# Kernel optimization log

Hardware: AMD Instinct MI355X
Metric: run time of the kernel (lower is better)

The kernel has to match this reference:

```python
import jax, jax.numpy as jnp
import numpy as np

N_NODES = 50000
N_EDGES = 800000
HID = 64
F_NODE = 64
F_EDGE = 16
DEC_H = 64
EPS = 1e-5


def setup_inputs() -> dict:
    key = jax.random.key(0)
    ks = jax.random.split(key, 16)
    inp = {}
    inp['x'] = jax.random.normal(ks[0], (N_NODES, F_NODE), dtype=jnp.float32)
    inp['edge_index'] = jax.random.randint(ks[1], (2, N_EDGES), 0, N_NODES, dtype=jnp.int32)
    inp['edge_attr'] = jax.random.normal(ks[2], (N_EDGES, F_EDGE), dtype=jnp.float32)
    # 3 GCN layers (F_NODE == HID so weights stack)
    inp['conv_w'] = jax.random.normal(ks[3], (3, HID, HID), dtype=jnp.float32) / np.sqrt(HID)
    inp['conv_b'] = jnp.zeros((3, HID), dtype=jnp.float32)
    inp['ln_g'] = jnp.ones((3, HID), dtype=jnp.float32)
    inp['ln_b'] = jnp.zeros((3, HID), dtype=jnp.float32)
    dec_in = 2 * HID + F_EDGE
    inp['dec_w1'] = jax.random.normal(ks[4], (dec_in, DEC_H), dtype=jnp.float32) / np.sqrt(dec_in)
    inp['dec_b1'] = jnp.zeros((DEC_H,), dtype=jnp.float32)
    inp['dec_w2'] = jax.random.normal(ks[5], (DEC_H, DEC_H // 2), dtype=jnp.float32) / np.sqrt(DEC_H)
    inp['dec_b2'] = jnp.zeros((DEC_H // 2,), dtype=jnp.float32)
    inp['dec_w3'] = jax.random.normal(ks[6], (DEC_H // 2, 1), dtype=jnp.float32) / np.sqrt(DEC_H // 2)
    inp['dec_b3'] = jnp.zeros((1,), dtype=jnp.float32)
    return inp


def _layer_norm(h, g, b):
    mu = jnp.mean(h, axis=-1, keepdims=True)
    var = jnp.mean(jnp.square(h - mu), axis=-1, keepdims=True)
    return (h - mu) * jax.lax.rsqrt(var + EPS) * g + b


def _forward(x, edge_index, edge_attr, conv_w, conv_b, ln_g, ln_b,
             dec_w1, dec_b1, dec_w2, dec_b2, dec_w3, dec_b3):
    n = x.shape[0]
    src, dst = edge_index[0], edge_index[1]
    # add self-loops (PyG GCNConv default)
    loop = jnp.arange(n, dtype=edge_index.dtype)
    src_sl = jnp.concatenate([src, loop])
    dst_sl = jnp.concatenate([dst, loop])
    # symmetric normalization: deg over target column (incl. self-loops)
    deg = jax.ops.segment_sum(jnp.ones_like(src_sl, dtype=x.dtype), dst_sl, num_segments=n)
    dinv = jnp.where(deg > 0, jax.lax.rsqrt(deg), 0.0)
    norm = dinv[src_sl] * dinv[dst_sl]  # (E+N,)

    h = x
    for l in range(conv_w.shape[0]):
        t = h @ conv_w[l]                                   # (N, H)
        msg = t[src_sl] * norm[:, None]                     # (E+N, H)
        agg = jax.ops.segment_sum(msg, dst_sl, num_segments=n) + conv_b[l]
        h = jax.nn.relu(_layer_norm(agg, ln_g[l], ln_b[l]))
        # dropout is identity at inference

    # edge decoder: concat(src_emb, dst_emb, edge_attr) -> MLP -> scalar
    z = jnp.concatenate([h[src], h[dst], edge_attr], axis=-1)  # (E, 2H+Fe)
    z = jax.nn.relu(z @ dec_w1 + dec_b1)
    z = jax.nn.relu(z @ dec_w2 + dec_b2)
    return (z @ dec_w3 + dec_b3).squeeze(-1)                   # (E,)


def reference(x, edge_index, edge_attr, conv_w, conv_b, ln_g, ln_b,
              dec_w1, dec_b1, dec_w2, dec_b2, dec_w3, dec_b3):
    return _forward(x, edge_index, edge_attr, conv_w, conv_b, ln_g, ln_b,
                    dec_w1, dec_b1, dec_w2, dec_b2, dec_w3, dec_b3)
```

## Files before the change

### kernel.cpp

```cpp
#include <hip/hip_runtime.h>
#include <hip/hip_fp16.h>

#define N_NODES 50000
#define N_EDGES 800000
#define HID 64
#define F_EDGE 16
#define LN_EPS 1e-5f
#define SCAN_BLOCKS ((N_NODES + 255) / 256)

typedef _Float16 h2n __attribute__((ext_vector_type(2)));

__device__ inline h2n to_n(__half2 v) {
    union { __half2 a; h2n b; } u; u.a = v; return u.b;
}
__device__ inline h2n pack2(float x, float y) {
    h2n r; r.x = (_Float16)x; r.y = (_Float16)y; return r;
}

__device__ inline float wave_sum64(float v) {
    #pragma unroll
    for (int o = 32; o > 0; o >>= 1) v += __shfl_xor(v, o, 64);
    return v;
}

__global__ void k_zero_cnt(int* __restrict__ cnt) {
    int i = blockIdx.x * blockDim.x + threadIdx.x;
    if (i < N_NODES) cnt[i] = 0;
}

__global__ void k_count(const int* __restrict__ dst, int* __restrict__ cnt) {
    int e = blockIdx.x * blockDim.x + threadIdx.x;
    if (e < N_EDGES) atomicAdd(&cnt[dst[e]], 1);
}

__global__ void k_scan1(const int* __restrict__ cnt, int* __restrict__ row_ptr,
                        int* __restrict__ bsum, float* __restrict__ dinv) {
    __shared__ int wsum[4];
    int tid = threadIdx.x, lane = tid & 63, w = tid >> 6;
    int i = blockIdx.x * 256 + tid;
    int v = (i < N_NODES) ? cnt[i] : 0;
    if (i < N_NODES) dinv[i] = rsqrtf((float)v + 1.0f);
    int isc = v;
    #pragma unroll
    for (int o = 1; o < 64; o <<= 1) {
        int n = __shfl_up(isc, o, 64);
        if (lane >= o) isc += n;
    }
    if (lane == 63) wsum[w] = isc;
    __syncthreads();
    int woff = 0;
    #pragma unroll
    for (int k = 0; k < 4; k++) woff += (k < w) ? wsum[k] : 0;
    if (i < N_NODES) row_ptr[i] = woff + isc - v;
    if (tid == 255) bsum[blockIdx.x] = woff + isc;
}

__global__ void k_scan2_prep(const int* __restrict__ bsum, int* __restrict__ boff,
                             const float* __restrict__ W1c, const float* __restrict__ W2,
                             __half2* __restrict__ w1cp, __half2* __restrict__ w2p) {
    __shared__ int wsum[4];
    int tid = threadIdx.x, lane = tid & 63, w = tid >> 6;
    int v = (tid < SCAN_BLOCKS) ? bsum[tid] : 0;
    int isc = v;
    #pragma unroll
    for (int o = 1; o < 64; o <<= 1) {
        int n = __shfl_up(isc, o, 64);
        if (lane >= o) isc += n;
    }
    if (lane == 63) wsum[w] = isc;
    __syncthreads();
    int woff = 0;
    #pragma unroll
    for (int k = 0; k < 4; k++) woff += (k < w) ? wsum[k] : 0;
    if (tid < SCAN_BLOCKS) boff[tid] = woff + isc - v;
    for (int i = tid; i < 8 * 64; i += 256) {
        int k2 = i >> 6, j = i & 63;
        w1cp[i] = __floats2half2_rn(W1c[(2 * k2) * 64 + j], W1c[(2 * k2 + 1) * 64 + j]);
    }
    for (int i = tid; i < 32 * 32; i += 256) {
        int k2 = i >> 5, j = i & 31;
        w2p[i] = __floats2half2_rn(W2[(2 * k2) * 32 + j], W2[(2 * k2 + 1) * 32 + j]);
    }
}

__global__ void k_scan3(int* __restrict__ row_ptr, const int* __restrict__ boff,
                        int* __restrict__ cursor) {
    int i = blockIdx.x * blockDim.x + threadIdx.x;
    if (i < N_NODES) {
        int r = row_ptr[i] + boff[i >> 8];
        row_ptr[i] = r;
        cursor[i] = r;
    }
    if (i == 0) row_ptr[N_NODES] = N_EDGES;
}

__global__ void k_fill(const int* __restrict__ src, const int* __restrict__ dst,
                       int* __restrict__ cursor, int* __restrict__ col) {
    int e = blockIdx.x * blockDim.x + threadIdx.x;
    if (e < N_EDGES) {
        int s = src[e], d = dst[e];
        int pos = atomicAdd(&cursor[d], 1);
        col[pos] = s;
    }
}

__global__ void k_xs_init(const float* __restrict__ x, const float* __restrict__ dinv,
                          __half* __restrict__ xs) {
    int i = blockIdx.x * blockDim.x + threadIdx.x;
    if (i < N_NODES * 64) xs[i] = __float2half_rn(x[i] * dinv[i >> 6]);
}

__device__ inline void row_acc(float4 raw, float m, float acc[8]) {
    const __half2* hp = (const __half2*)&raw;
    float2 f0 = __half22float2(hp[0]);
    float2 f1 = __half22float2(hp[1]);
    float2 f2 = __half22float2(hp[2]);
    float2 f3 = __half22float2(hp[3]);
    acc[0] = fmaf(f0.x, m, acc[0]); acc[1] = fmaf(f0.y, m, acc[1]);
    acc[2] = fmaf(f1.x, m, acc[2]); acc[3] = fmaf(f1.y, m, acc[3]);
    acc[4] = fmaf(f2.x, m, acc[4]); acc[5] = fmaf(f2.y, m, acc[5]);
    acc[6] = fmaf(f3.x, m, acc[6]); acc[7] = fmaf(f3.y, m, acc[7]);
}

__global__ void __launch_bounds__(256)
k_gather_agg(const __half* __restrict__ xs, const float* __restrict__ dinv,
             const int* __restrict__ row_ptr, const int* __restrict__ col,
             float* __restrict__ agg) {
    int gid = blockIdx.x * blockDim.x + threadIdx.x;
    int n = gid >> 3;
    if (n >= N_NODES) return;
    int c8 = gid & 7;
    const float4* x4 = (const float4*)xs;

    float acc[8];
    {
        float4 raw = x4[(size_t)n * 8 + c8];
        const __half2* hp = (const __half2*)&raw;
        float2 f0 = __half22float2(hp[0]);
        float2 f1 = __half22float2(hp[1]);
        float2 f2 = __half22float2(hp[2]);
        float2 f3 = __half22float2(hp[3]);
        acc[0] = f0.x; acc[1] = f0.y; acc[2] = f1.x; acc[3] = f1.y;
        acc[4] = f2.x; acc[5] = f2.y; acc[6] = f3.x; acc[7] = f3.y;
    }

    int beg = row_ptr[n], end = row_ptr[n + 1];
    int t = beg;
    int s0 = 0, s1 = 0, s2 = 0, s3 = 0;
    if (t < end) {
        int e1 = end - 1;
        s0 = col[t];
        s1 = col[min(t + 1, e1)];
        s2 = col[min(t + 2, e1)];
        s3 = col[min(t + 3, e1)];
    }
    while (t < end) {
        float m1 = (t + 1 < end) ? 1.0f : 0.0f;
        float m2 = (t + 2 < end) ? 1.0f : 0.0f;
        float m3 = (t + 3 < end) ? 1.0f : 0.0f;
        float4 r0 = x4[(size_t)s0 * 8 + c8];
        float4 r1 = x4[(size_t)s1 * 8 + c8];
        float4 r2 = x4[(size_t)s2 * 8 + c8];
        float4 r3 = x4[(size_t)s3 * 8 + c8];
        t += 4;
        if (t < end) {
            int e1 = end - 1;
            s0 = col[t];
            s1 = col[min(t + 1, e1)];
            s2 = col[min(t + 2, e1)];
            s3 = col[min(t + 3, e1)];
        }
        row_acc(r0, 1.0f, acc);
        row_acc(r1, m1, acc);
        row_acc(r2, m2, acc);
        row_acc(r3, m3, acc);
    }

    float di = dinv[n];
    float4 y0, y1;
    y0.x = acc[0] * di; y0.y = acc[1] * di; y0.z = acc[2] * di; y0.w = acc[3] * di;
    y1.x = acc[4] * di; y1.y = acc[5] * di; y1.z = acc[6] * di; y1.w = acc[7] * di;
    float4* a4 = (float4*)agg;
    a4[(size_t)n * 16 + 2 * c8] = y0;
    a4[(size_t)n * 16 + 2 * c8 + 1] = y1;
}

__global__ void __launch_bounds__(256)
k_gemm_ln(const float* __restrict__ agg, const float* __restrict__ W,
          const float* __restrict__ cb, const float* __restrict__ g,
          const float* __restrict__ b, const float* __restrict__ dinv,
          __half* __restrict__ xs_out, float* __restrict__ h_out) {
    int lane = threadIdx.x & 63;
    int wid = (blockIdx.x * blockDim.x + threadIdx.x) >> 6;
    int nwaves = (gridDim.x * blockDim.x) >> 6;
    float w[64];
    #pragma unroll
    for (int k = 0; k < 64; k++) w[k] = W[k * 64 + lane];
    float cbl = cb[lane], gl = g[lane], bl = b[lane];
    for (int row = wid; row < N_NODES; row += nwaves) {
        int r = __builtin_amdgcn_readfirstlane(row);
        const float* xr = agg + r * 64;
        float acc = cbl;
        #pragma unroll
        for (int k = 0; k < 64; k++) acc = fmaf(xr[k], w[k], acc);
        float mu = wave_sum64(acc) * (1.0f / 64.0f);
        float d = acc - mu;
        float var = wave_sum64(d * d) * (1.0f / 64.0f);
        float y = fmaxf(fmaf(d * rsqrtf(var + LN_EPS), gl, bl), 0.0f);
        if (xs_out) {
            xs_out[r * 64 + lane] = __float2half_rn(y * dinv[r]);
        } else {
            h_out[r * 64 + lane] = y;
        }
    }
}

__global__ void __launch_bounds__(256)
k_gemm_pq(const float* __restrict__ hin, const float* __restrict__ Wp,
          const float* __restrict__ bp, const float* __restrict__ Wq,
          __half* __restrict__ P, __half* __restrict__ Q) {
    int half_g = gridDim.x >> 1;
    bool isQ = (blockIdx.x >= half_g);
    const float* W = isQ ? Wq : Wp;
    __half* out = isQ ? Q : P;
    int lane = threadIdx.x & 63;
    int bid = isQ ? (blockIdx.x - half_g) : blockIdx.x;
    int wid = (bid * blockDim.x + threadIdx.x) >> 6;
    int nwaves = (half_g * blockDim.x) >> 6;
    float w[64];
    #pragma unroll
    for (int k = 0; k < 64; k++) w[k] = W[k * 64 + lane];
    float binit = isQ ? 0.0f : bp[lane];
    for (int row = wid; row < N_NODES; row += nwaves) {
        int r = __builtin_amdgcn_readfirstlane(row);
        const float* xr = hin + r * 64;
        float acc = binit;
        #pragma unroll
        for (int k = 0; k < 64; k++) acc = fmaf(xr[k], w[k], acc);
        out[r * 64 + lane] = __float2half_rn(acc);
    }
}

__global__ void __launch_bounds__(256)
k_decoder(const __half* __restrict__ P, const __half* __restrict__ Q,
          const int* __restrict__ src, const int* __restrict__ dst,
          const float* __restrict__ attr,
          const __half2* __restrict__ w1cp,
          const __half2* __restrict__ w2p, const float* __restrict__ b2,
          const float* __restrict__ W3, const float* __restrict__ b3,
          float* __restrict__ out) {
    int e = blockIdx.x * blockDim.x + threadIdx.x;
    if (e >= N_EDGES) return;
    int s = src[e], d = dst[e];

    const float4* ap = (const float4*)(attr + (size_t)e * 16);
    float4 av0 = ap[0], av1 = ap[1], av2 = ap[2], av3 = ap[3];
    h2n a2[8];
    a2[0] = pack2(av0.x, av0.y); a2[1] = pack2(av0.z, av0.w);
    a2[2] = pack2(av1.x, av1.y); a2[3] = pack2(av1.z, av1.w);
    a2[4] = pack2(av2.x, av2.y); a2[5] = pack2(av2.z, av2.w);
    a2[6] = pack2(av3.x, av3.y); a2[7] = pack2(av3.z, av3.w);

    float acc[64];
    const float4* Pp = (const float4*)(P + (size_t)s * 64);
    const float4* Qp = (const float4*)(Q + (size_t)d * 64);
    #pragma unroll
    for (int c = 0; c < 8; c++) {
        float4 pv = Pp[c], qv = Qp[c];
        const __half2* ph = (const __half2*)&pv;
        const __half2* qh = (const __half2*)&qv;
        #pragma unroll
        for (int u = 0; u < 4; u++) {
            float2 pf = __half22float2(ph[u]);
            float2 qf = __half22float2(qh[u]);
            acc[8 * c + 2 * u]     = pf.x + qf.x;
            acc[8 * c + 2 * u + 1] = pf.y + qf.y;
        }
    }

    #pragma unroll
    for (int k2 = 0; k2 < 8; k2++) {
        #pragma unroll
        for (int j = 0; j < 64; j++)
            acc[j] = __builtin_amdgcn_fdot2(a2[k2], to_n(w1cp[k2 * 64 + j]), acc[j], false);
    }

    h2n hh[32];
    #pragma unroll
    for (int k2 = 0; k2 < 32; k2++)
        hh[k2] = pack2(fmaxf(acc[2 * k2], 0.0f), fmaxf(acc[2 * k2 + 1], 0.0f));

    float acc2[32];
    #pragma unroll
    for (int j = 0; j < 32; j++) acc2[j] = b2[j];
    #pragma unroll
    for (int k2 = 0; k2 < 32; k2++) {
        #pragma unroll
        for (int j = 0; j < 32; j++)
            acc2[j] = __builtin_amdgcn_fdot2(hh[k2], to_n(w2p[k2 * 32 + j]), acc2[j], false);
    }

    float o = b3[0];
    #pragma unroll
    for (int j = 0; j < 32; j++)
        o = fmaf(fmaxf(acc2[j], 0.0f), W3[j], o);
    out[e] = o;
}

extern "C" void kernel_launch(void* const* d_in, const int* in_sizes, int n_in,
                              void* d_out, int out_size, void* d_ws, size_t ws_size,
                              hipStream_t stream) {
    const float* x      = (const float*)d_in[0];
    const int*   ei     = (const int*)d_in[1];
    const float* attr   = (const float*)d_in[2];
    const float* conv_w = (const float*)d_in[3];
    const float* conv_b = (const float*)d_in[4];
    const float* ln_g   = (const float*)d_in[5];
    const float* ln_b   = (const float*)d_in[6];
    const float* dw1    = (const float*)d_in[7];
    const float* db1    = (const float*)d_in[8];
    const float* dw2    = (const float*)d_in[9];
    const float* db2    = (const float*)d_in[10];
    const float* dw3    = (const float*)d_in[11];
    const float* db3    = (const float*)d_in[12];
    float* out = (float*)d_out;

    const int* src = ei;
    const int* dst = ei + N_EDGES;

    char* p = (char*)d_ws;
    float*   dinv    = (float*)p;   p += sizeof(float) * N_NODES;
    float*   agg     = (float*)p;   p += sizeof(float) * (size_t)N_NODES * 64;
    float*   h3      = (float*)p;   p += sizeof(float) * (size_t)N_NODES * 64;
    __half*  xs      = (__half*)p;  p += sizeof(__half) * (size_t)N_NODES * 64;
    __half*  P_h     = (__half*)p;  p += sizeof(__half) * (size_t)N_NODES * 64;
    __half*  Q_h     = (__half*)p;  p += sizeof(__half) * (size_t)N_NODES * 64;
    int*     cnt     = (int*)p;     p += sizeof(int) * N_NODES;
    int*     cursor  = (int*)p;     p += sizeof(int) * N_NODES;
    int*     row_ptr = (int*)p;     p += sizeof(int) * (N_NODES + 1);
    int*     col     = (int*)p;     p += sizeof(int) * N_EDGES;
    int*     bsum    = (int*)p;     p += sizeof(int) * 256;
    int*     boff    = (int*)p;     p += sizeof(int) * 256;
    __half2* w1cp    = (__half2*)p; p += sizeof(__half2) * 8 * 64;
    __half2* w2p     = (__half2*)p; p += sizeof(__half2) * 32 * 32;

    const int nb_nodes = (N_NODES + 255) / 256;
    const int nb_edges = (N_EDGES + 255) / 256;
    const int nb_elems = (N_NODES * 64 + 255) / 256;

    k_zero_cnt<<<nb_nodes, 256, 0, stream>>>(cnt);
    k_count<<<nb_edges, 256, 0, stream>>>(dst, cnt);
    k_scan1<<<SCAN_BLOCKS, 256, 0, stream>>>(cnt, row_ptr, bsum, dinv);
    k_scan2_prep<<<1, 256, 0, stream>>>(bsum, boff, dw1 + 128 * 64, dw2, w1cp, w2p);
    k_scan3<<<nb_nodes, 256, 0, stream>>>(row_ptr, boff, cursor);
    k_fill<<<nb_edges, 256, 0, stream>>>(src, dst, cursor, col);
    k_xs_init<<<nb_elems, 256, 0, stream>>>(x, dinv, xs);

    const int gemm_blocks = 1024;
    const int gather_blocks = (N_NODES * 8 + 255) / 256;

    for (int l = 0; l < 3; l++) {
        k_gather_agg<<<gather_blocks, 256, 0, stream>>>(xs, dinv, row_ptr, col, agg);
        bool last = (l == 2);
        k_gemm_ln<<<gemm_blocks, 256, 0, stream>>>(
            agg, conv_w + l * 4096, conv_b + l * 64,
            ln_g + l * 64, ln_b + l * 64, dinv,
            last ? (__half*)nullptr : xs, last ? h3 : (float*)nullptr);
    }

    k_gemm_pq<<<2 * gemm_blocks, 256, 0, stream>>>(h3, dw1, db1, dw1 + 64 * 64, P_h, Q_h);

    k_decoder<<<nb_edges, 256, 0, stream>>>(
        P_h, Q_h, src, dst, attr, w1cp, w2p, db2, dw3, db3, out);
}
```

Baseline: 438.8 us.

## Process decoder edges in CSR order and fuse setup kernels

The decoder now walks edges in destination-sorted CSR order, using a new eid permutation array written by k_fill, so Q rows (by dst) are reused across neighbouring threads and gathers get better cache locality. Attr reads and output writes become scattered through eid, which is the cost paid for that locality. The xs initialisation is folded into the scan3 kernel and the count-zeroing kernel is replaced by a memset, cutting two launches.

```diff
diff --git a/kernel.cpp b/kernel.cpp
--- a/kernel.cpp
+++ b/kernel.cpp
@@ -21,11 +21,6 @@
     #pragma unroll
     for (int o = 32; o > 0; o >>= 1) v += __shfl_xor(v, o, 64);
     return v;
-}
-
-__global__ void k_zero_cnt(int* __restrict__ cnt) {
-    int i = blockIdx.x * blockDim.x + threadIdx.x;
-    if (i < N_NODES) cnt[i] = 0;
 }
 
 __global__ void k_count(const int* __restrict__ dst, int* __restrict__ cnt) {
@@ -83,8 +78,10 @@
     }
 }
 
-__global__ void k_scan3(int* __restrict__ row_ptr, const int* __restrict__ boff,
-                        int* __restrict__ cursor) {
+__global__ void k_scan3_xs(int* __restrict__ row_ptr, const int* __restrict__ boff,
+                           int* __restrict__ cursor,
+                           const float* __restrict__ x, const float* __restrict__ dinv,
+                           __half* __restrict__ xs) {
     int i = blockIdx.x * blockDim.x + threadIdx.x;
     if (i < N_NODES) {
         int r = row_ptr[i] + boff[i >> 8];
@@ -92,22 +89,19 @@
         cursor[i] = r;
     }
     if (i == 0) row_ptr[N_NODES] = N_EDGES;
+    if (i < N_NODES * 64) xs[i] = __float2half_rn(x[i] * dinv[i >> 6]);
 }
 
 __global__ void k_fill(const int* __restrict__ src, const int* __restrict__ dst,
-                       int* __restrict__ cursor, int* __restrict__ col) {
+                       int* __restrict__ cursor, int* __restrict__ col,
+                       int* __restrict__ eid) {
     int e = blockIdx.x * blockDim.x + threadIdx.x;
     if (e < N_EDGES) {
         int s = src[e], d = dst[e];
         int pos = atomicAdd(&cursor[d], 1);
         col[pos] = s;
-    }
-}
-
-__global__ void k_xs_init(const float* __restrict__ x, const float* __restrict__ dinv,
-                          __half* __restrict__ xs) {
-    int i = blockIdx.x * blockDim.x + threadIdx.x;
-    if (i < N_NODES * 64) xs[i] = __float2half_rn(x[i] * dinv[i >> 6]);
+        eid[pos] = e;
+    }
 }
 
 __device__ inline void row_acc(float4 raw, float m, float acc[8]) {
@@ -243,15 +237,18 @@
 
 __global__ void __launch_bounds__(256)
 k_decoder(const __half* __restrict__ P, const __half* __restrict__ Q,
-          const int* __restrict__ src, const int* __restrict__ dst,
+          const int* __restrict__ col, const int* __restrict__ eid,
+          const int* __restrict__ dst,
           const float* __restrict__ attr,
           const __half2* __restrict__ w1cp,
           const __half2* __restrict__ w2p, const float* __restrict__ b2,
           const float* __restrict__ W3, const float* __restrict__ b3,
           float* __restrict__ out) {
-    int e = blockIdx.x * blockDim.x + threadIdx.x;
-    if (e >= N_EDGES) return;
-    int s = src[e], d = dst[e];
+    int p = blockIdx.x * blockDim.x + threadIdx.x;
+    if (p >= N_EDGES) return;
+    int s = col[p];
+    int e = eid[p];
+    int d = dst[e];
 
     const float4* ap = (const float4*)(attr + (size_t)e * 16);
     float4 av0 = ap[0], av1 = ap[1], av2 = ap[2], av3 = ap[3];
@@ -339,22 +336,21 @@
     int*     cursor  = (int*)p;     p += sizeof(int) * N_NODES;
     int*     row_ptr = (int*)p;     p += sizeof(int) * (N_NODES + 1);
     int*     col     = (int*)p;     p += sizeof(int) * N_EDGES;
+    int*     eid     = (int*)p;     p += sizeof(int) * N_EDGES;
     int*     bsum    = (int*)p;     p += sizeof(int) * 256;
     int*     boff    = (int*)p;     p += sizeof(int) * 256;
     __half2* w1cp    = (__half2*)p; p += sizeof(__half2) * 8 * 64;
     __half2* w2p     = (__half2*)p; p += sizeof(__half2) * 32 * 32;
 
-    const int nb_nodes = (N_NODES + 255) / 256;
     const int nb_edges = (N_EDGES + 255) / 256;
     const int nb_elems = (N_NODES * 64 + 255) / 256;
 
-    k_zero_cnt<<<nb_nodes, 256, 0, stream>>>(cnt);
+    hipMemsetAsync(cnt, 0, sizeof(int) * N_NODES, stream);
     k_count<<<nb_edges, 256, 0, stream>>>(dst, cnt);
     k_scan1<<<SCAN_BLOCKS, 256, 0, stream>>>(cnt, row_ptr, bsum, dinv);
     k_scan2_prep<<<1, 256, 0, stream>>>(bsum, boff, dw1 + 128 * 64, dw2, w1cp, w2p);
-    k_scan3<<<nb_nodes, 256, 0, stream>>>(row_ptr, boff, cursor);
-    k_fill<<<nb_edges, 256, 0, stream>>>(src, dst, cursor, col);
-    k_xs_init<<<nb_elems, 256, 0, stream>>>(x, dinv, xs);
+    k_scan3_xs<<<nb_elems, 256, 0, stream>>>(row_ptr, boff, cursor, x, dinv, xs);
+    k_fill<<<nb_edges, 256, 0, stream>>>(src, dst, cursor, col, eid);
 
     const int gemm_blocks = 1024;
     const int gather_blocks = (N_NODES * 8 + 255) / 256;
@@ -371,5 +367,5 @@
     k_gemm_pq<<<2 * gemm_blocks, 256, 0, stream>>>(h3, dw1, db1, dw1 + 64 * 64, P_h, Q_h);
 
     k_decoder<<<nb_edges, 256, 0, stream>>>(
-        P_h, Q_h, src, dst, attr, w1cp, w2p, db2, dw3, db3, out);
-}
+        P_h, Q_h, col, eid, dst, attr, w1cp, w2p, db2, dw3, db3, out);
+}
```

Measured after the change: 437.0 us. No clear change (-0.4%).

## Split neighbor gather into two source-range passes for cache locality

Applied to the files above, without the earlier changes.

Each node's CSR row is partitioned by source index (below or above the midpoint), recorded with a packed high/low count and a second fill cursor. Aggregation then runs as two passes, each touching only half of the feature table, so that the gathered working set fits better in cache. The second pass reloads the partial sums and applies the normalization. Separately, the count zeroing is replaced by a memset and the xs init is fused into the scan3 kernel. The cost is an extra launch per layer and an extra read/write of agg.

```diff
diff --git a/kernel.cpp b/kernel.cpp
--- a/kernel.cpp
+++ b/kernel.cpp
@@ -3,12 +3,14 @@
 
 #define N_NODES 50000
 #define N_EDGES 800000
+#define MID 25000
 #define HID 64
 #define F_EDGE 16
 #define LN_EPS 1e-5f
 #define SCAN_BLOCKS ((N_NODES + 255) / 256)
 
 typedef _Float16 h2n __attribute__((ext_vector_type(2)));
+typedef float f4 __attribute__((ext_vector_type(4)));
 
 __device__ inline h2n to_n(__half2 v) {
     union { __half2 a; h2n b; } u; u.a = v; return u.b;
@@ -23,14 +25,13 @@
     return v;
 }
 
-__global__ void k_zero_cnt(int* __restrict__ cnt) {
-    int i = blockIdx.x * blockDim.x + threadIdx.x;
-    if (i < N_NODES) cnt[i] = 0;
-}
-
-__global__ void k_count(const int* __restrict__ dst, int* __restrict__ cnt) {
+__global__ void k_count(const int* __restrict__ src, const int* __restrict__ dst,
+                        int* __restrict__ cnt) {
     int e = blockIdx.x * blockDim.x + threadIdx.x;
-    if (e < N_EDGES) atomicAdd(&cnt[dst[e]], 1);
+    if (e < N_EDGES) {
+        int s = src[e], d = dst[e];
+        atomicAdd(&cnt[d], (s < MID) ? 0x10001 : 1);
+    }
 }
 
 __global__ void k_scan1(const int* __restrict__ cnt, int* __restrict__ row_ptr,
@@ -38,7 +39,7 @@
     __shared__ int wsum[4];
     int tid = threadIdx.x, lane = tid & 63, w = tid >> 6;
     int i = blockIdx.x * 256 + tid;
-    int v = (i < N_NODES) ? cnt[i] : 0;
+    int v = (i < N_NODES) ? (cnt[i] & 0xffff) : 0;
     if (i < N_NODES) dinv[i] = rsqrtf((float)v + 1.0f);
     int isc = v;
     #pragma unroll
@@ -83,31 +84,35 @@
     }
 }
 
-__global__ void k_scan3(int* __restrict__ row_ptr, const int* __restrict__ boff,
-                        int* __restrict__ cursor) {
+__global__ void k_scan3_xs(int* __restrict__ row_ptr, const int* __restrict__ boff,
+                           const int* __restrict__ cnt,
+                           int* __restrict__ cursor, int* __restrict__ cursor2,
+                           int* __restrict__ split,
+                           const float* __restrict__ x, const float* __restrict__ dinv,
+                           __half* __restrict__ xs) {
     int i = blockIdx.x * blockDim.x + threadIdx.x;
     if (i < N_NODES) {
         int r = row_ptr[i] + boff[i >> 8];
         row_ptr[i] = r;
         cursor[i] = r;
+        int sp = r + (cnt[i] >> 16);
+        split[i] = sp;
+        cursor2[i] = sp;
     }
     if (i == 0) row_ptr[N_NODES] = N_EDGES;
+    if (i < N_NODES * 64) xs[i] = __float2half_rn(x[i] * dinv[i >> 6]);
 }
 
 __global__ void k_fill(const int* __restrict__ src, const int* __restrict__ dst,
-                       int* __restrict__ cursor, int* __restrict__ col) {
+                       int* __restrict__ cursor, int* __restrict__ cursor2,
+                       int* __restrict__ col) {
     int e = blockIdx.x * blockDim.x + threadIdx.x;
     if (e < N_EDGES) {
         int s = src[e], d = dst[e];
-        int pos = atomicAdd(&cursor[d], 1);
+        int pos = (s < MID) ? atomicAdd(&cursor[d], 1)
+                            : atomicAdd(&cursor2[d], 1);
         col[pos] = s;
     }
-}
-
-__global__ void k_xs_init(const float* __restrict__ x, const float* __restrict__ dinv,
-                          __half* __restrict__ xs) {
-    int i = blockIdx.x * blockDim.x + threadIdx.x;
-    if (i < N_NODES * 64) xs[i] = __float2half_rn(x[i] * dinv[i >> 6]);
 }
 
 __device__ inline void row_acc(float4 raw, float m, float acc[8]) {
@@ -124,16 +129,20 @@
 
 __global__ void __launch_bounds__(256)
 k_gather_agg(const __half* __restrict__ xs, const float* __restrict__ dinv,
-             const int* __restrict__ row_ptr, const int* __restrict__ col,
-             float* __restrict__ agg) {
+             const int* __restrict__ row_ptr, const int* __restrict__ split,
+             const int* __restrict__ col, float* __restrict__ agg, int pass) {
     int gid = blockIdx.x * blockDim.x + threadIdx.x;
     int n = gid >> 3;
     if (n >= N_NODES) return;
     int c8 = gid & 7;
     const float4* x4 = (const float4*)xs;
 
+    int beg, end; bool self;
+    if (pass == 0) { beg = row_ptr[n]; end = split[n];       self = (n <  MID); }
+    else           { beg = split[n];   end = row_ptr[n + 1]; self = (n >= MID); }
+
     float acc[8];
-    {
+    if (self) {
         float4 raw = x4[(size_t)n * 8 + c8];
         const __half2* hp = (const __half2*)&raw;
         float2 f0 = __half22float2(hp[0]);
@@ -142,9 +151,11 @@
         float2 f3 = __half22float2(hp[3]);
         acc[0] = f0.x; acc[1] = f0.y; acc[2] = f1.x; acc[3] = f1.y;
         acc[4] = f2.x; acc[5] = f2.y; acc[6] = f3.x; acc[7] = f3.y;
-    }
-
-    int beg = row_ptr[n], end = row_ptr[n + 1];
+    } else {
+        #pragma unroll
+        for (int u = 0; u < 8; u++) acc[u] = 0.0f;
+    }
+
     int t = beg;
     int s0 = 0, s1 = 0, s2 = 0, s3 = 0;
     if (t < end) {
@@ -176,13 +187,26 @@
         row_acc(r3, m3, acc);
     }
 
-    float di = dinv[n];
-    float4 y0, y1;
-    y0.x = acc[0] * di; y0.y = acc[1] * di; y0.z = acc[2] * di; y0.w = acc[3] * di;
-    y1.x = acc[4] * di; y1.y = acc[5] * di; y1.z = acc[6] * di; y1.w = acc[7] * di;
-    float4* a4 = (float4*)agg;
-    a4[(size_t)n * 16 + 2 * c8] = y0;
-    a4[(size_t)n * 16 + 2 * c8 + 1] = y1;
+    f4* a4 = (f4*)agg;
+    size_t base = (size_t)n * 16 + 2 * c8;
+    if (pass == 0) {
+        f4 y0, y1;
+        y0.x = acc[0]; y0.y = acc[1]; y0.z = acc[2]; y0.w = acc[3];
+        y1.x = acc[4]; y1.y = acc[5]; y1.z = acc[6]; y1.w = acc[7];
+        __builtin_nontemporal_store(y0, &a4[base]);
+        __builtin_nontemporal_store(y1, &a4[base + 1]);
+    } else {
+        f4 p0 = __builtin_nontemporal_load(&a4[base]);
+        f4 p1 = __builtin_nontemporal_load(&a4[base + 1]);
+        float di = dinv[n];
+        f4 y0, y1;
+        y0.x = (acc[0] + p0.x) * di; y0.y = (acc[1] + p0.y) * di;
+        y0.z = (acc[2] + p0.z) * di; y0.w = (acc[3] + p0.w) * di;
+        y1.x = (acc[4] + p1.x) * di; y1.y = (acc[5] + p1.y) * di;
+        y1.z = (acc[6] + p1.z) * di; y1.w = (acc[7] + p1.w) * di;
+        a4[base] = y0;
+        a4[base + 1] = y1;
+    }
 }
 
 __global__ void __launch_bounds__(256)
@@ -337,6 +361,8 @@
     __half*  Q_h     = (__half*)p;  p += sizeof(__half) * (size_t)N_NODES * 64;
     int*     cnt     = (int*)p;     p += sizeof(int) * N_NODES;
     int*     cursor  = (int*)p;     p += sizeof(int) * N_NODES;
+    int*     cursor2 = (int*)p;     p += sizeof(int) * N_NODES;
+    int*     split   = (int*)p;     p += sizeof(int) * N_NODES;
     int*     row_ptr = (int*)p;     p += sizeof(int) * (N_NODES + 1);
     int*     col     = (int*)p;     p += sizeof(int) * N_EDGES;
     int*     bsum    = (int*)p;     p += sizeof(int) * 256;
@@ -344,23 +370,23 @@
     __half2* w1cp    = (__half2*)p; p += sizeof(__half2) * 8 * 64;
     __half2* w2p     = (__half2*)p; p += sizeof(__half2) * 32 * 32;
 
-    const int nb_nodes = (N_NODES + 255) / 256;
     const int nb_edges = (N_EDGES + 255) / 256;
     const int nb_elems = (N_NODES * 64 + 255) / 256;
 
-    k_zero_cnt<<<nb_nodes, 256, 0, stream>>>(cnt);
-    k_count<<<nb_edges, 256, 0, stream>>>(dst, cnt);
+    (void)hipMemsetAsync(cnt, 0, sizeof(int) * N_NODES, stream);
+    k_count<<<nb_edges, 256, 0, stream>>>(src, dst, cnt);
     k_scan1<<<SCAN_BLOCKS, 256, 0, stream>>>(cnt, row_ptr, bsum, dinv);
     k_scan2_prep<<<1, 256, 0, stream>>>(bsum, boff, dw1 + 128 * 64, dw2, w1cp, w2p);
-    k_scan3<<<nb_nodes, 256, 0, stream>>>(row_ptr, boff, cursor);
-    k_fill<<<nb_edges, 256, 0, stream>>>(src, dst, cursor, col);
-    k_xs_init<<<nb_elems, 256, 0, stream>>>(x, dinv, xs);
+    k_scan3_xs<<<nb_elems, 256, 0, stream>>>(row_ptr, boff, cnt, cursor, cursor2,
+                                             split, x, dinv, xs);
+    k_fill<<<nb_edges, 256, 0, stream>>>(src, dst, cursor, cursor2, col);
 
     const int gemm_blocks = 1024;
     const int gather_blocks = (N_NODES * 8 + 255) / 256;
 
     for (int l = 0; l < 3; l++) {
-        k_gather_agg<<<gather_blocks, 256, 0, stream>>>(xs, dinv, row_ptr, col, agg);
+        k_gather_agg<<<gather_blocks, 256, 0, stream>>>(xs, dinv, row_ptr, split, col, agg, 0);
+        k_gather_agg<<<gather_blocks, 256, 0, stream>>>(xs, dinv, row_ptr, split, col, agg, 1);
         bool last = (l == 2);
         k_gemm_ln<<<gemm_blocks, 256, 0, stream>>>(
             agg, conv_w + l * 4096, conv_b + l * 64,
```

New measurement: 483.6 us. 10.2% more time.

## Fuse GCN gather-aggregate with GEMM+LayerNorm per layer via LDS tile

Applied to the files above, without the earlier changes.

Merges the per-layer neighbor gather-aggregate kernel and the dense GEMM+LayerNorm kernel into one kernel. Each wave aggregates 8 nodes into a swizzled shared-memory tile, then runs the 64x64 matvec and LayerNorm from that tile. This removes the float32 agg round trip through global memory and three launches, and ping-pongs between two half-precision feature buffers. It also folds the xs initialisation into the scan3 kernel and replaces the zero kernel with a memset. In exchange, every wave now reloads all 64 weight columns per 8 rows, which raises register pressure and per-row load overhead.

```diff
diff --git a/kernel.cpp b/kernel.cpp
--- a/kernel.cpp
+++ b/kernel.cpp
@@ -21,11 +21,6 @@
     #pragma unroll
     for (int o = 32; o > 0; o >>= 1) v += __shfl_xor(v, o, 64);
     return v;
-}
-
-__global__ void k_zero_cnt(int* __restrict__ cnt) {
-    int i = blockIdx.x * blockDim.x + threadIdx.x;
-    if (i < N_NODES) cnt[i] = 0;
 }
 
 __global__ void k_count(const int* __restrict__ dst, int* __restrict__ cnt) {
@@ -83,8 +78,10 @@
     }
 }
 
-__global__ void k_scan3(int* __restrict__ row_ptr, const int* __restrict__ boff,
-                        int* __restrict__ cursor) {
+__global__ void k_scan3_xs(int* __restrict__ row_ptr, const int* __restrict__ boff,
+                           int* __restrict__ cursor,
+                           const float* __restrict__ x, const float* __restrict__ dinv,
+                           __half* __restrict__ xs) {
     int i = blockIdx.x * blockDim.x + threadIdx.x;
     if (i < N_NODES) {
         int r = row_ptr[i] + boff[i >> 8];
@@ -92,6 +89,7 @@
         cursor[i] = r;
     }
     if (i == 0) row_ptr[N_NODES] = N_EDGES;
+    if (i < N_NODES * 64) xs[i] = __float2half_rn(x[i] * dinv[i >> 6]);
 }
 
 __global__ void k_fill(const int* __restrict__ src, const int* __restrict__ dst,
@@ -102,12 +100,6 @@
         int pos = atomicAdd(&cursor[d], 1);
         col[pos] = s;
     }
-}
-
-__global__ void k_xs_init(const float* __restrict__ x, const float* __restrict__ dinv,
-                          __half* __restrict__ xs) {
-    int i = blockIdx.x * blockDim.x + threadIdx.x;
-    if (i < N_NODES * 64) xs[i] = __float2half_rn(x[i] * dinv[i >> 6]);
 }
 
 __device__ inline void row_acc(float4 raw, float m, float acc[8]) {
@@ -123,14 +115,20 @@
 }
 
 __global__ void __launch_bounds__(256)
-k_gather_agg(const __half* __restrict__ xs, const float* __restrict__ dinv,
-             const int* __restrict__ row_ptr, const int* __restrict__ col,
-             float* __restrict__ agg) {
-    int gid = blockIdx.x * blockDim.x + threadIdx.x;
-    int n = gid >> 3;
-    if (n >= N_NODES) return;
-    int c8 = gid & 7;
-    const float4* x4 = (const float4*)xs;
+k_layer(const __half* __restrict__ xs_in, const float* __restrict__ dinv,
+        const int* __restrict__ row_ptr, const int* __restrict__ col,
+        const float* __restrict__ W, const float* __restrict__ cb,
+        const float* __restrict__ gW, const float* __restrict__ bW,
+        __half* __restrict__ xs_out, float* __restrict__ h_out) {
+    __shared__ __align__(16) float tile[4][8 * 68];
+    int tid = threadIdx.x;
+    int wv = tid >> 6, lane = tid & 63;
+    int base = (blockIdx.x * 4 + wv) * 8;
+    if (base >= N_NODES) return;
+    int g8 = lane >> 3;
+    int c8 = lane & 7;
+    int n = base + g8;
+    const float4* x4 = (const float4*)xs_in;
 
     float acc[8];
     {
@@ -143,7 +141,6 @@
         acc[0] = f0.x; acc[1] = f0.y; acc[2] = f1.x; acc[3] = f1.y;
         acc[4] = f2.x; acc[5] = f2.y; acc[6] = f3.x; acc[7] = f3.y;
     }
-
     int beg = row_ptr[n], end = row_ptr[n + 1];
     int t = beg;
     int s0 = 0, s1 = 0, s2 = 0, s3 = 0;
@@ -176,41 +173,46 @@
         row_acc(r3, m3, acc);
     }
 
-    float di = dinv[n];
-    float4 y0, y1;
-    y0.x = acc[0] * di; y0.y = acc[1] * di; y0.z = acc[2] * di; y0.w = acc[3] * di;
-    y1.x = acc[4] * di; y1.y = acc[5] * di; y1.z = acc[6] * di; y1.w = acc[7] * di;
-    float4* a4 = (float4*)agg;
-    a4[(size_t)n * 16 + 2 * c8] = y0;
-    a4[(size_t)n * 16 + 2 * c8 + 1] = y1;
-}
-
-__global__ void __launch_bounds__(256)
-k_gemm_ln(const float* __restrict__ agg, const float* __restrict__ W,
-          const float* __restrict__ cb, const float* __restrict__ g,
-          const float* __restrict__ b, const float* __restrict__ dinv,
-          __half* __restrict__ xs_out, float* __restrict__ h_out) {
-    int lane = threadIdx.x & 63;
-    int wid = (blockIdx.x * blockDim.x + threadIdx.x) >> 6;
-    int nwaves = (gridDim.x * blockDim.x) >> 6;
+    {
+        float di = dinv[n];
+        float4 y0, y1;
+        y0.x = acc[0] * di; y0.y = acc[1] * di; y0.z = acc[2] * di; y0.w = acc[3] * di;
+        y1.x = acc[4] * di; y1.y = acc[5] * di; y1.z = acc[6] * di; y1.w = acc[7] * di;
+        float4* rowv = (float4*)&tile[wv][g8 * 68];
+        rowv[(2 * c8)     ^ (g8 << 1)] = y0;
+        rowv[(2 * c8 + 1) ^ (g8 << 1)] = y1;
+    }
+
     float w[64];
     #pragma unroll
     for (int k = 0; k < 64; k++) w[k] = W[k * 64 + lane];
-    float cbl = cb[lane], gl = g[lane], bl = b[lane];
-    for (int row = wid; row < N_NODES; row += nwaves) {
-        int r = __builtin_amdgcn_readfirstlane(row);
-        const float* xr = agg + r * 64;
-        float acc = cbl;
-        #pragma unroll
-        for (int k = 0; k < 64; k++) acc = fmaf(xr[k], w[k], acc);
-        float mu = wave_sum64(acc) * (1.0f / 64.0f);
-        float d = acc - mu;
+    float cbl = cb[lane], gl = gW[lane], bl = bW[lane];
+    #pragma unroll
+    for (int r = 0; r < 8; r++) {
+        const float4* rw = (const float4*)&tile[wv][r * 68];
+        float a = cbl;
+        #pragma unroll
+        for (int j = 0; j < 8; j++) {
+            float4 p0 = rw[(2 * j)     ^ (r << 1)];
+            float4 p1 = rw[(2 * j + 1) ^ (r << 1)];
+            a = fmaf(p0.x, w[j * 8 + 0], a);
+            a = fmaf(p0.y, w[j * 8 + 1], a);
+            a = fmaf(p0.z, w[j * 8 + 2], a);
+            a = fmaf(p0.w, w[j * 8 + 3], a);
+            a = fmaf(p1.x, w[j * 8 + 4], a);
+            a = fmaf(p1.y, w[j * 8 + 5], a);
+            a = fmaf(p1.z, w[j * 8 + 6], a);
+            a = fmaf(p1.w, w[j * 8 + 7], a);
+        }
+        float mu = wave_sum64(a) * (1.0f / 64.0f);
+        float d = a - mu;
         float var = wave_sum64(d * d) * (1.0f / 64.0f);
         float y = fmaxf(fmaf(d * rsqrtf(var + LN_EPS), gl, bl), 0.0f);
+        int nr = base + r;
         if (xs_out) {
-            xs_out[r * 64 + lane] = __float2half_rn(y * dinv[r]);
+            xs_out[nr * 64 + lane] = __float2half_rn(y * dinv[nr]);
         } else {
-            h_out[r * 64 + lane] = y;
+            h_out[nr * 64 + lane] = y;
         }
     }
 }
@@ -330,9 +332,9 @@
 
     char* p = (char*)d_ws;
     float*   dinv    = (float*)p;   p += sizeof(float) * N_NODES;
-    float*   agg     = (float*)p;   p += sizeof(float) * (size_t)N_NODES * 64;
     float*   h3      = (float*)p;   p += sizeof(float) * (size_t)N_NODES * 64;
-    __half*  xs      = (__half*)p;  p += sizeof(__half) * (size_t)N_NODES * 64;
+    __half*  xs_a    = (__half*)p;  p += sizeof(__half) * (size_t)N_NODES * 64;
+    __half*  xs_b    = (__half*)p;  p += sizeof(__half) * (size_t)N_NODES * 64;
     __half*  P_h     = (__half*)p;  p += sizeof(__half) * (size_t)N_NODES * 64;
     __half*  Q_h     = (__half*)p;  p += sizeof(__half) * (size_t)N_NODES * 64;
     int*     cnt     = (int*)p;     p += sizeof(int) * N_NODES;
@@ -344,29 +346,28 @@
     __half2* w1cp    = (__half2*)p; p += sizeof(__half2) * 8 * 64;
     __half2* w2p     = (__half2*)p; p += sizeof(__half2) * 32 * 32;
 
-    const int nb_nodes = (N_NODES + 255) / 256;
     const int nb_edges = (N_EDGES + 255) / 256;
     const int nb_elems = (N_NODES * 64 + 255) / 256;
 
-    k_zero_cnt<<<nb_nodes, 256, 0, stream>>>(cnt);
+    (void)hipMemsetAsync(cnt, 0, sizeof(int) * N_NODES, stream);
     k_count<<<nb_edges, 256, 0, stream>>>(dst, cnt);
     k_scan1<<<SCAN_BLOCKS, 256, 0, stream>>>(cnt, row_ptr, bsum, dinv);
     k_scan2_prep<<<1, 256, 0, stream>>>(bsum, boff, dw1 + 128 * 64, dw2, w1cp, w2p);
-    k_scan3<<<nb_nodes, 256, 0, stream>>>(row_ptr, boff, cursor);
+    k_scan3_xs<<<nb_elems, 256, 0, stream>>>(row_ptr, boff, cursor, x, dinv, xs_a);
     k_fill<<<nb_edges, 256, 0, stream>>>(src, dst, cursor, col);
-    k_xs_init<<<nb_elems, 256, 0, stream>>>(x, dinv, xs);
-
+
+    const int layer_blocks = (N_NODES / 8 + 3) / 4;
     const int gemm_blocks = 1024;
-    const int gather_blocks = (N_NODES * 8 + 255) / 256;
-
-    for (int l = 0; l < 3; l++) {
-        k_gather_agg<<<gather_blocks, 256, 0, stream>>>(xs, dinv, row_ptr, col, agg);
-        bool last = (l == 2);
-        k_gemm_ln<<<gemm_blocks, 256, 0, stream>>>(
-            agg, conv_w + l * 4096, conv_b + l * 64,
-            ln_g + l * 64, ln_b + l * 64, dinv,
-            last ? (__half*)nullptr : xs, last ? h3 : (float*)nullptr);
-    }
+
+    k_layer<<<layer_blocks, 256, 0, stream>>>(
+        xs_a, dinv, row_ptr, col, conv_w + 0 * 4096, conv_b + 0 * 64,
+        ln_g + 0 * 64, ln_b + 0 * 64, xs_b, (float*)nullptr);
+    k_layer<<<layer_blocks, 256, 0, stream>>>(
+        xs_b, dinv, row_ptr, col, conv_w + 1 * 4096, conv_b + 1 * 64,
+        ln_g + 1 * 64, ln_b + 1 * 64, xs_a, (float*)nullptr);
+    k_layer<<<layer_blocks, 256, 0, stream>>>(
+        xs_a, dinv, row_ptr, col, conv_w + 2 * 4096, conv_b + 2 * 64,
+        ln_g + 2 * 64, ln_b + 2 * 64, (__half*)nullptr, h3);
 
     k_gemm_pq<<<2 * gemm_blocks, 256, 0, stream>>>(h3, dw1, db1, dw1 + 64 * 64, P_h, Q_h);
 
```

New measurement: 415.7 us. 5.2% less time.
